# Kernel tuning notes

Hardware: AMD Instinct MI355X
Metric: run time of the kernel (lower is better)

The kernel has to match this reference:

```python
import jax, jax.numpy as jnp
import numpy as np

B, S, D, H = 4, 4096, 1024, 128

def setup_inputs() -> dict:
    key = jax.random.key(0)
    k1, k2, k3, k4 = jax.random.split(key, 4)
    scale = 1.0 / np.sqrt(D)
    return {
        "x": jax.random.normal(k1, (B, S, D), dtype=jnp.float32),
        "Wq": jax.random.normal(k2, (H, D), dtype=jnp.float32) * scale,
        "Wk": jax.random.normal(k3, (H, D), dtype=jnp.float32) * scale,
        "Wv": jax.random.normal(k4, (H, D), dtype=jnp.float32) * scale,
    }

def reference(x, Wq, Wk, Wv):
    # Linear(in,out,bias=False): y = x @ W.T
    q = jnp.einsum('bsd,hd->bsh', x, Wq)
    k = jnp.einsum('bsd,hd->bsh', x, Wk)
    v = jnp.einsum('bsd,hd->bsh', x, Wv)
    scores = jnp.einsum('bqh,bkh->bqk', q, k) / jnp.sqrt(jnp.float32(H))
    num_toks = x.shape[1]
    causal = jnp.tril(jnp.ones((num_toks, num_toks), dtype=bool))
    scores = jnp.where(causal[None, :, :], scores, -jnp.inf)
    probs = jax.nn.softmax(scores, axis=-1)
    return jnp.einsum('bqk,bkh->bqh', probs, v)
```

## Files before the change

kernel.cpp:

```cpp
#include <hip/hip_runtime.h>
#include <hip/hip_bf16.h>

#define BATCH  4
#define SEQ    4096
#define DMODEL 1024
#define HDIM   128
#define MROWS  (BATCH * SEQ)
#define NT32   (SEQ / 32)
#define T32    (BATCH * NT32)
#define NS     4

#define BM 64
#define BN 96
#define BK 64
#define KT (DMODEL / BK)

typedef __attribute__((ext_vector_type(8)))  short short8;
typedef __attribute__((ext_vector_type(4)))  float floatx4;
typedef __attribute__((ext_vector_type(16))) float floatx16;
typedef unsigned int u32;

static __device__ __forceinline__ short f2bf(float f) {
    __hip_bfloat16 h = __float2bfloat16(f);
    union { __hip_bfloat16 h; short s; } u; u.h = h;
    return u.s;
}

static __device__ __forceinline__ float bf2f(unsigned short s) {
    union { u32 u; float f; } v; v.u = ((u32)s) << 16;
    return v.f;
}

static __device__ __forceinline__ short8 ld8(const unsigned short* p) {
    return *reinterpret_cast<const short8*>(p);
}

static __device__ __forceinline__ u32 cvtpk_bf16(float a, float b) {
    u32 r;
    asm("v_cvt_pk_bf16_f32 %0, %1, %2" : "=v"(r) : "v"(a), "v"(b));
    return r;
}

static __device__ __forceinline__ void swap_halves(u32& a, u32& b) {
#if __has_builtin(__builtin_amdgcn_permlane32_swap)
    typedef __attribute__((ext_vector_type(2))) int int2v;
    int2v r = __builtin_amdgcn_permlane32_swap((int)a, (int)b, false, false);
    a = (u32)r[0]; b = (u32)r[1];
#else
    u32 ap = (u32)__shfl_xor((int)a, 32);
    u32 bp = (u32)__shfl_xor((int)b, 32);
    const bool hih = (threadIdx.x & 32) != 0;
    u32 na = hih ? bp : a;
    u32 nb = hih ? b : ap;
    a = na; b = nb;
#endif
}


__global__ __launch_bounds__(256) void cvt_w_kernel(
    const float* __restrict__ Wq, const float* __restrict__ Wk,
    const float* __restrict__ Wv, unsigned short* __restrict__ wbt)
{
    const int n8w = HDIM * DMODEL / 8;
    int i = blockIdx.x * 256 + threadIdx.x;
    if (i >= 3 * n8w) return;
    const int which = i / n8w;
    const int j = i - which * n8w;
    const float* src = (which == 0) ? Wq : (which == 1) ? Wk : Wv;
    const float scale = (which == 0) ? 0.08838834764831845f : 1.0f;
    const float4* s4 = reinterpret_cast<const float4*>(src);
    float4 a = s4[2 * j];
    float4 b = s4[2 * j + 1];
    short8 o;
    o[0] = f2bf(a.x * scale); o[1] = f2bf(a.y * scale);
    o[2] = f2bf(a.z * scale); o[3] = f2bf(a.w * scale);
    o[4] = f2bf(b.x * scale); o[5] = f2bf(b.y * scale);
    o[6] = f2bf(b.z * scale); o[7] = f2bf(b.w * scale);
    const int n  = which * HDIM + (j >> 7);
    const int k0 = (j & 127) * 8;
    const size_t addr =
        ((size_t)((n >> 4) * 32 + (k0 >> 5)) << 9)
        + (((n & 15) + (((k0 >> 3) & 3) * 16)) * 8);
    *reinterpret_cast<short8*>(wbt + addr) = o;
}

__global__ __launch_bounds__(256, 4) void qkv_kernel(
    const float* __restrict__ x,
    const unsigned short* __restrict__ wbt,
    unsigned short* __restrict__ qt,
    unsigned short* __restrict__ kt,
    unsigned short* __restrict__ vtl)
{
    __shared__ __align__(16) unsigned short A_lds[2][BM][BK];

    const int raw  = blockIdx.x;
    const int vid  = (raw & 7) * 128 + (raw >> 3);
    const int mblk = vid >> 2;
    const int nblk = vid & 3;
    const int m0   = mblk * BM;
    const int n0   = nblk * BN;
    const int nb0  = n0 >> 4;

    const int tid  = threadIdx.x;
    const int wv   = tid >> 6;
    const int lane = tid & 63;
    const int lr   = lane & 15;
    const int lh   = lane >> 4;
    const int wm   = wv >> 1;
    const int wn   = wv & 1;

    const int ar = tid >> 2;
    const int aq = tid & 3;
    const float* asrc = x + (size_t)(m0 + ar) * DMODEL + aq * 16;

    floatx4 acc[2][3];
#pragma unroll
    for (int mf = 0; mf < 2; ++mf)
#pragma unroll
        for (int nf = 0; nf < 3; ++nf) acc[mf][nf] = (floatx4){0.f, 0.f, 0.f, 0.f};

    {
        float4 f0 = *reinterpret_cast<const float4*>(asrc);
        float4 f1 = *reinterpret_cast<const float4*>(asrc + 4);
        float4 f2 = *reinterpret_cast<const float4*>(asrc + 8);
        float4 f3 = *reinterpret_cast<const float4*>(asrc + 12);
        short8 v0, v1;
        v0[0] = f2bf(f0.x); v0[1] = f2bf(f0.y); v0[2] = f2bf(f0.z); v0[3] = f2bf(f0.w);
        v0[4] = f2bf(f1.x); v0[5] = f2bf(f1.y); v0[6] = f2bf(f1.z); v0[7] = f2bf(f1.w);
        v1[0] = f2bf(f2.x); v1[1] = f2bf(f2.y); v1[2] = f2bf(f2.z); v1[3] = f2bf(f2.w);
        v1[4] = f2bf(f3.x); v1[5] = f2bf(f3.y); v1[6] = f2bf(f3.z); v1[7] = f2bf(f3.w);
        const int u0 = (2 * aq)     ^ (ar & 7);
        const int u1 = (2 * aq + 1) ^ (ar & 7);
        *reinterpret_cast<short8*>(&A_lds[0][ar][u0 * 8]) = v0;
        *reinterpret_cast<short8*>(&A_lds[0][ar][u1 * 8]) = v1;
    }
    __syncthreads();

    for (int ktile = 0; ktile < KT; ++ktile) {
        const int cur = ktile & 1;
        const int nxt = cur ^ 1;
        float4 f0, f1, f2, f3;
        if (ktile + 1 < KT) {
            const float* a = asrc + (ktile + 1) * BK;
            f0 = *reinterpret_cast<const float4*>(a);
            f1 = *reinterpret_cast<const float4*>(a + 4);
            f2 = *reinterpret_cast<const float4*>(a + 8);
            f3 = *reinterpret_cast<const float4*>(a + 12);
        }
#pragma unroll
        for (int kk = 0; kk < 2; ++kk) {
            const int uswz   = (kk * 4 + lh) ^ (lr & 7);
            const int kchunk = ktile * 2 + kk;
            short8 af[2], bfr[3];
#pragma unroll
            for (int mf = 0; mf < 2; ++mf)
                af[mf] = ld8(&A_lds[cur][wm * 32 + mf * 16 + lr][uswz * 8]);
#pragma unroll
            for (int nf = 0; nf < 3; ++nf)
                bfr[nf] = ld8(wbt
                    + ((size_t)((nb0 + wn * 3 + nf) * 32 + kchunk) << 9)
                    + lane * 8);
#pragma unroll
            for (int mf = 0; mf < 2; ++mf)
#pragma unroll
                for (int nf = 0; nf < 3; ++nf)
                    acc[mf][nf] = __builtin_amdgcn_mfma_f32_16x16x32_bf16(
                        af[mf], bfr[nf], acc[mf][nf], 0, 0, 0);
        }
        if (ktile + 1 < KT) {
            short8 v0, v1;
            v0[0] = f2bf(f0.x); v0[1] = f2bf(f0.y); v0[2] = f2bf(f0.z); v0[3] = f2bf(f0.w);
            v0[4] = f2bf(f1.x); v0[5] = f2bf(f1.y); v0[6] = f2bf(f1.z); v0[7] = f2bf(f1.w);
            v1[0] = f2bf(f2.x); v1[1] = f2bf(f2.y); v1[2] = f2bf(f2.z); v1[3] = f2bf(f2.w);
            v1[4] = f2bf(f3.x); v1[5] = f2bf(f3.y); v1[6] = f2bf(f3.z); v1[7] = f2bf(f3.w);
            const int u0 = (2 * aq)     ^ (ar & 7);
            const int u1 = (2 * aq + 1) ^ (ar & 7);
            *reinterpret_cast<short8*>(&A_lds[nxt][ar][u0 * 8]) = v0;
            *reinterpret_cast<short8*>(&A_lds[nxt][ar][u1 * 8]) = v1;
        }
        __syncthreads();
    }

    __syncthreads();
    unsigned short* out_l = &A_lds[0][0][0];

    const int t0 = (m0 & (SEQ - 1)) >> 5;
    const int bb = m0 >> 12;
    const int st = wm;

#pragma unroll
    for (int nf = 0; nf < 3; ++nf) {
        const int cl = wn * 48 + nf * 16 + lr;
#pragma unroll
        for (int mf = 0; mf < 2; ++mf) {
#pragma unroll
            for (int r = 0; r < 4; ++r) {
                const int srow = mf * 16 + lh * 4 + r;
                const unsigned short vv = (unsigned short)f2bf(acc[mf][nf][r]);
                int lf, off;
                if (nblk == 0) {
                    lf  = st * 6 + (cl >> 4);
                    off = ((cl >> 3) & 1) * 256 + srow * 8 + (cl & 7);
                } else if (nblk == 1) {
                    lf  = (cl < 32) ? st * 6 + (cl >> 4)
                                    : st * 6 + 2 + ((cl - 32) >> 4);
                    off = ((cl >> 3) & 1) * 256 + srow * 8 + (cl & 7);
                } else if (nblk == 2) {
                    if (cl < 64) {
                        lf  = st * 6 + (cl >> 4);
                        off = ((cl >> 3) & 1) * 256 + srow * 8 + (cl & 7);
                    } else {
                        const int dg = cl - 64;
                        lf  = st * 6 + 4 + ((srow >> 4) & 1);
                        off = ((srow >> 3) & 1) * 256 + dg * 8 + (srow & 7);
                    }
                } else {
                    const int d = cl + 32;
                    lf  = st * 6 + ((d >> 5) - 1) * 2 + ((srow >> 4) & 1);
                    off = ((srow >> 3) & 1) * 256 + (d & 31) * 8 + (srow & 7);
                }
                out_l[lf * 512 + off] = vv;
            }
        }
    }
    __syncthreads();

#pragma unroll
    for (int k = 0; k < 3; ++k) {
        const int u   = tid + 256 * k;
        const int fb  = u >> 6;
        const int iu  = u & 63;
        const int fst = (fb >= 6) ? 1 : 0;
        const int li  = fb - 6 * fst;
        const size_t tb8 = (size_t)((bb * NT32 + t0 + fst) * 8);
        unsigned short* gbase;
        if (nblk == 0) {
            gbase = qt + ((tb8 + li) << 9);
        } else if (nblk == 1) {
            gbase = (li < 2) ? qt  + ((tb8 + 6 + li) << 9)
                             : kt  + ((tb8 + (li - 2)) << 9);
        } else if (nblk == 2) {
            gbase = (li < 4) ? kt  + ((tb8 + 4 + li) << 9)
                             : vtl + ((tb8 + (li - 4)) << 9);
        } else {
            gbase = vtl + ((tb8 + 2 + li) << 9);
        }
        *reinterpret_cast<short8*>(gbase + iu * 8) =
            *reinterpret_cast<const short8*>(&out_l[fb * 512 + iu * 8]);
    }
}

__global__ __launch_bounds__(64) void attn_kernel(
    const unsigned short* __restrict__ qt,
    const unsigned short* __restrict__ kt,
    const unsigned short* __restrict__ vtl,
    unsigned short* __restrict__ pacc,
    float* __restrict__ pm,
    float* __restrict__ pl)
{
    const int bid  = blockIdx.x;
    const int xcd  = bid & 7;
    const int b    = xcd >> 1;
    const int par  = xcd & 1;
    const int idx  = bid >> 3;
    const int s    = idx & 3;
    const int trk  = idx >> 2;
    const int t32b = (NT32 - 1) - (trk * 2 + par);
    const int q0   = t32b * 32;
    const int t32  = b * NT32 + t32b;
    const int lane = threadIdx.x & 63;
    const int l31  = lane & 31;
    const int hih  = lane >> 5;

    const int nkv   = q0 + 32;
    const int chunk = ((nkv + NS * 32 - 1) / (NS * 32)) * 32;
    const int lo    = s * chunk;
    const int hikv  = (lo + chunk < nkv) ? lo + chunk : nkv;
    const size_t mlbase = (size_t)(s * T32 + t32) * 32;

    if (lo >= hikv) {
        if (lane < 32) { pm[mlbase + l31] = -3.0e38f; pl[mlbase + l31] = 0.f; }
        return;
    }

    const unsigned short* qtb =
        qt + ((size_t)((b * NT32 + t32b) * 8) << 9) + lane * 8;
    short8 qa[8];
#pragma unroll
    for (int ks = 0; ks < 8; ++ks) qa[ks] = ld8(qtb + (ks << 9));

    const unsigned short* ktbase = kt  + ((size_t)(b * NT32 * 8) << 9) + lane * 8;
    const unsigned short* vtbase = vtl + ((size_t)(b * NT32 * 8) << 9) + lane * 8;

    floatx16 acco[4];
#pragma unroll
    for (int db = 0; db < 4; ++db)
#pragma unroll
        for (int i = 0; i < 16; ++i) acco[db][i] = 0.f;
    float m_r = -3.0e38f, l_r = 0.f;

    short8 kf[8];
#pragma unroll
    for (int ks = 0; ks < 8; ++ks)
        kf[ks] = ld8(ktbase + ((size_t)((lo >> 5) * 8 + ks) << 9));

    for (int kv0 = lo; kv0 < hikv; kv0 += 32) {
        const int t = kv0 >> 5;
        const unsigned short* vtb = vtbase + ((size_t)(t * 8) << 9);

        short8 vf[8];
#pragma unroll
        for (int j = 0; j < 8; ++j) vf[j] = ld8(vtb + (j << 9));

        floatx16 sc;
#pragma unroll
        for (int i = 0; i < 16; ++i) sc[i] = 0.f;
        __builtin_amdgcn_s_setprio(1);
#pragma unroll
        for (int ks = 0; ks < 8; ++ks)
            sc = __builtin_amdgcn_mfma_f32_32x32x16_bf16(kf[ks], qa[ks], sc, 0, 0, 0);
        __builtin_amdgcn_s_setprio(0);

        const int tn = (kv0 + 32 < hikv) ? t + 1 : t;
#pragma unroll
        for (int ks = 0; ks < 8; ++ks)
            kf[ks] = ld8(ktbase + ((size_t)(tn * 8 + ks) << 9));

        if (kv0 == q0) {
#pragma unroll
            for (int r = 0; r < 16; ++r) {
                const int kvloc = (r & 3) + 8 * (r >> 2) + 4 * hih;
                if (kvloc > l31) sc[r] = -3.0e38f;
            }
        }
        float t8[8];
#pragma unroll
        for (int i = 0; i < 8; ++i) t8[i] = fmaxf(sc[i], sc[i + 8]);
        float t4a = fmaxf(t8[0], t8[4]), t4b = fmaxf(t8[1], t8[5]);
        float t4c = fmaxf(t8[2], t8[6]), t4d = fmaxf(t8[3], t8[7]);
        float pmax = fmaxf(fmaxf(t4a, t4b), fmaxf(t4c, t4d));
        pmax = fmaxf(pmax, __shfl_xor(pmax, 32));
        if (__any(pmax > m_r + 8.f)) {
            const float mn  = fmaxf(m_r, pmax);
            const float fac = __expf(m_r - mn);
            m_r = mn; l_r *= fac;
#pragma unroll
            for (int db = 0; db < 4; ++db)
#pragma unroll
                for (int i = 0; i < 16; ++i) acco[db][i] *= fac;
        }
        float p[16];
#pragma unroll
        for (int r = 0; r < 16; ++r) p[r] = __expf(sc[r] - m_r);
        float s8[8];
#pragma unroll
        for (int i = 0; i < 8; ++i) s8[i] = p[i] + p[i + 8];
        float s4a = s8[0] + s8[4], s4b = s8[1] + s8[5];
        float s4c = s8[2] + s8[6], s4d = s8[3] + s8[7];
        float ps = (s4a + s4b) + (s4c + s4d);
        ps += __shfl_xor(ps, 32);
        l_r += ps;
        u32 pk0 = cvtpk_bf16(p[0], p[1]),   pk2 = cvtpk_bf16(p[4], p[5]);
        swap_halves(pk0, pk2);
        u32 pk1 = cvtpk_bf16(p[2], p[3]),   pk3 = cvtpk_bf16(p[6], p[7]);
        swap_halves(pk1, pk3);
        u32 pk4 = cvtpk_bf16(p[8], p[9]),   pk6 = cvtpk_bf16(p[12], p[13]);
        swap_halves(pk4, pk6);
        u32 pk5 = cvtpk_bf16(p[10], p[11]), pk7 = cvtpk_bf16(p[14], p[15]);
        swap_halves(pk5, pk7);
        union { u32 u[4]; short8 s8v; } ua, ub;
        ua.u[0] = pk0; ua.u[1] = pk1; ua.u[2] = pk2; ua.u[3] = pk3;
        ub.u[0] = pk4; ub.u[1] = pk5; ub.u[2] = pk6; ub.u[3] = pk7;
        const short8 pa0 = ua.s8v, pa1 = ub.s8v;
        __builtin_amdgcn_s_setprio(1);
#pragma unroll
        for (int db = 0; db < 4; ++db) {
            acco[db] = __builtin_amdgcn_mfma_f32_32x32x16_bf16(vf[2 * db],     pa0, acco[db], 0, 0, 0);
            acco[db] = __builtin_amdgcn_mfma_f32_32x32x16_bf16(vf[2 * db + 1], pa1, acco[db], 0, 0, 0);
        }
        __builtin_amdgcn_s_setprio(0);
    }

    unsigned short* pt = pacc + (size_t)(s * T32 + t32) * 128 * 32;
#pragma unroll
    for (int db = 0; db < 4; ++db)
#pragma unroll
        for (int r = 0; r < 16; ++r) {
            const int dloc = db * 32 + (r & 3) + 8 * (r >> 2) + 4 * hih;
            pt[(size_t)dloc * 32 + l31] = (unsigned short)f2bf(acco[db][r]);
        }
    if (lane < 32) { pm[mlbase + l31] = m_r; pl[mlbase + l31] = l_r; }
}

__global__ __launch_bounds__(256) void combine_kernel(
    const unsigned short* __restrict__ pacc, const float* __restrict__ pm,
    const float* __restrict__ pl, float* __restrict__ out)
{
    __shared__ float wlds[NS][32];
    __shared__ float tlds[128][33];
    const int t32 = blockIdx.x;
    const int tid = threadIdx.x;

    if (tid < 32) {
        const int q = tid;
        float ms[NS], ls[NS];
        float M = -3.0e38f;
#pragma unroll
        for (int s = 0; s < NS; ++s) {
            ms[s] = pm[(size_t)(s * T32 + t32) * 32 + q];
            ls[s] = pl[(size_t)(s * T32 + t32) * 32 + q];
            M = fmaxf(M, ms[s]);
        }
        float w[NS], den = 0.f;
#pragma unroll
        for (int s = 0; s < NS; ++s) { w[s] = __expf(ms[s] - M); den += w[s] * ls[s]; }
        const float inv = 1.f / den;
#pragma unroll
        for (int s = 0; s < NS; ++s) wlds[s][q] = w[s] * inv;
    }
    __syncthreads();

#pragma unroll
    for (int rep = 0; rep < 16; ++rep) {
        const int flat = rep * 256 + tid;
        const int d = flat >> 5, q = flat & 31;
        float acc = 0.f;
#pragma unroll
        for (int s = 0; s < NS; ++s)
            acc += wlds[s][q] *
                   bf2f(pacc[((size_t)(s * T32 + t32) * 128 + d) * 32 + q]);
        tlds[d][q] = acc;
    }
    __syncthreads();

    const size_t row0 = (size_t)t32 * 32;
#pragma unroll
    for (int rep = 0; rep < 16; ++rep) {
        const int flat = rep * 256 + tid;
        const int q = flat >> 7, d = flat & 127;
        out[(row0 + q) * 128 + d] = tlds[d][q];
    }
}

extern "C" void kernel_launch(void* const* d_in, const int* in_sizes, int n_in,
                              void* d_out, int out_size, void* d_ws, size_t ws_size,
                              hipStream_t stream)
{
    const float* x  = (const float*)d_in[0];
    const float* Wq = (const float*)d_in[1];
    const float* Wk = (const float*)d_in[2];
    const float* Wv = (const float*)d_in[3];
    float* out = (float*)d_out;

    const size_t TBUF = (size_t)BATCH * NT32 * 8 * 512;

    unsigned short* wbt  = (unsigned short*)d_ws;
    unsigned short* qt   = wbt + (size_t)384 * DMODEL;
    unsigned short* ktb  = qt + TBUF;
    unsigned short* vtl  = ktb + TBUF;
    unsigned short* pacc = vtl + TBUF;
    float* pm = (float*)(pacc + (size_t)NS * T32 * 128 * 32);
    float* pl = pm + (size_t)NS * T32 * 32;

    const int n8w3 = 3 * HDIM * DMODEL / 8;
    cvt_w_kernel<<<(n8w3 + 255) / 256, 256, 0, stream>>>(Wq, Wk, Wv, wbt);

    qkv_kernel<<<(MROWS / BM) * (384 / BN), 256, 0, stream>>>(x, wbt, qt, ktb, vtl);

    attn_kernel<<<T32 * NS, 64, 0, stream>>>(qt, ktb, vtl, pacc, pm, pl);

    combine_kernel<<<T32, 256, 0, stream>>>(pacc, pm, pl, out);
}
```

Baseline: 79.08 us.

## Pre-convert x to bf16 MFMA-tiled layout in a separate kernel

Adds a cvt_x_kernel that converts x from fp32 to bf16 once and writes it in the fragment-tiled layout MFMA expects. The QKV GEMM then loads A fragments straight from global memory, with no LDS staging, double buffering or per-tile syncthreads. This removes the repeated fp32 reads and conversions, since each x row was read by four N-blocks. In exchange it adds a kernel launch and a full bf16 write and read of x. The xat buffer shares workspace with pacc, which is safe only because attn writes pacc after qkv has consumed xat.

```diff
diff --git a/kernel.cpp b/kernel.cpp
--- a/kernel.cpp
+++ b/kernel.cpp
@@ -84,14 +84,50 @@
     *reinterpret_cast<short8*>(wbt + addr) = o;
 }
 
+__global__ __launch_bounds__(256) void cvt_x_kernel(
+    const float* __restrict__ x, unsigned short* __restrict__ xat)
+{
+    __shared__ __align__(16) unsigned short xl[16 * 1024];
+    const int mt  = blockIdx.x;
+    const int m0  = mt * 16;
+    const int tid = threadIdx.x;
+    const int r   = tid & 15;
+    const int c   = tid >> 4;
+    const float* src = x + (size_t)(m0 + r) * DMODEL + c * 64;
+#pragma unroll
+    for (int rep = 0; rep < 8; ++rep) {
+        float4 f0 = *reinterpret_cast<const float4*>(src + rep * 8);
+        float4 f1 = *reinterpret_cast<const float4*>(src + rep * 8 + 4);
+        short8 v;
+        v[0] = f2bf(f0.x); v[1] = f2bf(f0.y); v[2] = f2bf(f0.z); v[3] = f2bf(f0.w);
+        v[4] = f2bf(f1.x); v[5] = f2bf(f1.y); v[6] = f2bf(f1.z); v[7] = f2bf(f1.w);
+        const int ko = c * 8 + rep;
+        *reinterpret_cast<short8*>(&xl[r * 1024 + ((ko ^ (r & 7)) * 8)]) = v;
+    }
+    __syncthreads();
+    unsigned short* dst = xat + ((size_t)mt * 32) * 512;
+#pragma unroll
+    for (int rep = 0; rep < 8; ++rep) {
+        const int og  = rep * 256 + tid;
+        const int low = og & 63;
+        const int kc  = og >> 6;
+        const int r2  = low & 15;
+        const int c16 = low >> 4;
+        const int ko  = kc * 4 + c16;
+        short8 v = *reinterpret_cast<const short8*>(
+            &xl[r2 * 1024 + ((ko ^ (r2 & 7)) * 8)]);
+        *reinterpret_cast<short8*>(dst + og * 8) = v;
+    }
+}
+
 __global__ __launch_bounds__(256, 4) void qkv_kernel(
-    const float* __restrict__ x,
+    const unsigned short* __restrict__ xat,
     const unsigned short* __restrict__ wbt,
     unsigned short* __restrict__ qt,
     unsigned short* __restrict__ kt,
     unsigned short* __restrict__ vtl)
 {
-    __shared__ __align__(16) unsigned short A_lds[2][BM][BK];
+    __shared__ __align__(16) unsigned short out_l[6144];
 
     const int raw  = blockIdx.x;
     const int vid  = (raw & 7) * 128 + (raw >> 3);
@@ -99,6 +135,7 @@
     const int nblk = vid & 3;
     const int m0   = mblk * BM;
     const int n0   = nblk * BN;
+    const int mt0  = m0 >> 4;
     const int nb0  = n0 >> 4;
 
     const int tid  = threadIdx.x;
@@ -109,57 +146,28 @@
     const int wm   = wv >> 1;
     const int wn   = wv & 1;
 
-    const int ar = tid >> 2;
-    const int aq = tid & 3;
-    const float* asrc = x + (size_t)(m0 + ar) * DMODEL + aq * 16;
-
     floatx4 acc[2][3];
 #pragma unroll
     for (int mf = 0; mf < 2; ++mf)
 #pragma unroll
         for (int nf = 0; nf < 3; ++nf) acc[mf][nf] = (floatx4){0.f, 0.f, 0.f, 0.f};
 
-    {
-        float4 f0 = *reinterpret_cast<const float4*>(asrc);
-        float4 f1 = *reinterpret_cast<const float4*>(asrc + 4);
-        float4 f2 = *reinterpret_cast<const float4*>(asrc + 8);
-        float4 f3 = *reinterpret_cast<const float4*>(asrc + 12);
-        short8 v0, v1;
-        v0[0] = f2bf(f0.x); v0[1] = f2bf(f0.y); v0[2] = f2bf(f0.z); v0[3] = f2bf(f0.w);
-        v0[4] = f2bf(f1.x); v0[5] = f2bf(f1.y); v0[6] = f2bf(f1.z); v0[7] = f2bf(f1.w);
-        v1[0] = f2bf(f2.x); v1[1] = f2bf(f2.y); v1[2] = f2bf(f2.z); v1[3] = f2bf(f2.w);
-        v1[4] = f2bf(f3.x); v1[5] = f2bf(f3.y); v1[6] = f2bf(f3.z); v1[7] = f2bf(f3.w);
-        const int u0 = (2 * aq)     ^ (ar & 7);
-        const int u1 = (2 * aq + 1) ^ (ar & 7);
-        *reinterpret_cast<short8*>(&A_lds[0][ar][u0 * 8]) = v0;
-        *reinterpret_cast<short8*>(&A_lds[0][ar][u1 * 8]) = v1;
-    }
-    __syncthreads();
+    const unsigned short* abase = xat + lane * 8;
+    const unsigned short* bbase = wbt + lane * 8;
 
     for (int ktile = 0; ktile < KT; ++ktile) {
-        const int cur = ktile & 1;
-        const int nxt = cur ^ 1;
-        float4 f0, f1, f2, f3;
-        if (ktile + 1 < KT) {
-            const float* a = asrc + (ktile + 1) * BK;
-            f0 = *reinterpret_cast<const float4*>(a);
-            f1 = *reinterpret_cast<const float4*>(a + 4);
-            f2 = *reinterpret_cast<const float4*>(a + 8);
-            f3 = *reinterpret_cast<const float4*>(a + 12);
-        }
 #pragma unroll
         for (int kk = 0; kk < 2; ++kk) {
-            const int uswz   = (kk * 4 + lh) ^ (lr & 7);
             const int kchunk = ktile * 2 + kk;
             short8 af[2], bfr[3];
 #pragma unroll
             for (int mf = 0; mf < 2; ++mf)
-                af[mf] = ld8(&A_lds[cur][wm * 32 + mf * 16 + lr][uswz * 8]);
+                af[mf] = ld8(abase
+                    + ((size_t)((mt0 + wm * 2 + mf) * 32 + kchunk) << 9));
 #pragma unroll
             for (int nf = 0; nf < 3; ++nf)
-                bfr[nf] = ld8(wbt
-                    + ((size_t)((nb0 + wn * 3 + nf) * 32 + kchunk) << 9)
-                    + lane * 8);
+                bfr[nf] = ld8(bbase
+                    + ((size_t)((nb0 + wn * 3 + nf) * 32 + kchunk) << 9));
 #pragma unroll
             for (int mf = 0; mf < 2; ++mf)
 #pragma unroll
@@ -167,22 +175,7 @@
                     acc[mf][nf] = __builtin_amdgcn_mfma_f32_16x16x32_bf16(
                         af[mf], bfr[nf], acc[mf][nf], 0, 0, 0);
         }
-        if (ktile + 1 < KT) {
-            short8 v0, v1;
-            v0[0] = f2bf(f0.x); v0[1] = f2bf(f0.y); v0[2] = f2bf(f0.z); v0[3] = f2bf(f0.w);
-            v0[4] = f2bf(f1.x); v0[5] = f2bf(f1.y); v0[6] = f2bf(f1.z); v0[7] = f2bf(f1.w);
-            v1[0] = f2bf(f2.x); v1[1] = f2bf(f2.y); v1[2] = f2bf(f2.z); v1[3] = f2bf(f2.w);
-            v1[4] = f2bf(f3.x); v1[5] = f2bf(f3.y); v1[6] = f2bf(f3.z); v1[7] = f2bf(f3.w);
-            const int u0 = (2 * aq)     ^ (ar & 7);
-            const int u1 = (2 * aq + 1) ^ (ar & 7);
-            *reinterpret_cast<short8*>(&A_lds[nxt][ar][u0 * 8]) = v0;
-            *reinterpret_cast<short8*>(&A_lds[nxt][ar][u1 * 8]) = v1;
-        }
-        __syncthreads();
-    }
-
-    __syncthreads();
-    unsigned short* out_l = &A_lds[0][0][0];
+    }
 
     const int t0 = (m0 & (SEQ - 1)) >> 5;
     const int bb = m0 >> 12;
@@ -458,14 +451,17 @@
     unsigned short* qt   = wbt + (size_t)384 * DMODEL;
     unsigned short* ktb  = qt + TBUF;
     unsigned short* vtl  = ktb + TBUF;
-    unsigned short* pacc = vtl + TBUF;
+    unsigned short* xat  = vtl + TBUF;
+    unsigned short* pacc = xat;
     float* pm = (float*)(pacc + (size_t)NS * T32 * 128 * 32);
     float* pl = pm + (size_t)NS * T32 * 32;
 
     const int n8w3 = 3 * HDIM * DMODEL / 8;
     cvt_w_kernel<<<(n8w3 + 255) / 256, 256, 0, stream>>>(Wq, Wk, Wv, wbt);
 
-    qkv_kernel<<<(MROWS / BM) * (384 / BN), 256, 0, stream>>>(x, wbt, qt, ktb, vtl);
+    cvt_x_kernel<<<MROWS / 16, 256, 0, stream>>>(x, xat);
+
+    qkv_kernel<<<(MROWS / BM) * (384 / BN), 256, 0, stream>>>(xat, wbt, qt, ktb, vtl);
 
     attn_kernel<<<T32 * NS, 64, 0, stream>>>(qt, ktb, vtl, pacc, pm, pl);
 
```

Measured after the change: 87.63 us. 1.11x slower.
